# Performance work log

Hardware: AMD Instinct MI355X
Metric: run time of the kernel (lower is better)

## Reference

```python
import jax, jax.numpy as jnp
import numpy as np

N_IMG = 5
IN_DIM = 512
N_KERNEL = 200
KS = (2, 3, 5)
HIDDEN = 512
BATCH = 32768


def _param(key, shape, scale=0.02):
    return jax.random.normal(key, shape, dtype=jnp.float32) * scale


def setup_inputs() -> dict:
    key = jax.random.key(0)
    ks = jax.random.split(key, 16)
    feats = jax.random.normal(ks[0], (BATCH, N_IMG, IN_DIM), dtype=jnp.float32)
    d_cat = len(KS) * N_KERNEL  # 600
    return {
        "feats": feats,
        "w2": _param(ks[1], (N_KERNEL, 2, IN_DIM)), "b2": _param(ks[2], (N_KERNEL,)),
        "w3": _param(ks[3], (N_KERNEL, 3, IN_DIM)), "b3": _param(ks[4], (N_KERNEL,)),
        "w5": _param(ks[5], (N_KERNEL, 5, IN_DIM)), "b5": _param(ks[6], (N_KERNEL,)),
        "fc1_w": _param(ks[7], (d_cat, d_cat)), "fc1_b": _param(ks[8], (d_cat,)),
        "fc2_w": _param(ks[9], (d_cat, IN_DIM)), "fc2_b": _param(ks[10], (IN_DIM,)),
        "fc0_w": _param(ks[11], (2 * IN_DIM, HIDDEN)), "fc0_b": _param(ks[12], (HIDDEN,)),
        "fcs_w": _param(ks[13], (HIDDEN, 1)), "fcs_b": _param(ks[14], (1,)),
    }


def _conv_block(x, w, b):
    # x: [N, T, D], w: [C, K, D] -> relu(conv) then max over time -> [N, C]
    K = w.shape[1]
    T = x.shape[1] - K + 1
    win = jnp.stack([x[:, t:t + K, :] for t in range(T)], axis=1)  # [N, T, K, D]
    out = jnp.einsum('ntkd,ckd->ntc', win, w) + b                  # [N, T, C]
    return jnp.max(jax.nn.relu(out), axis=1)                       # [N, C]


def reference(feats, w2, b2, w3, b3, w5, b5, fc1_w, fc1_b, fc2_w, fc2_b,
              fc0_w, fc0_b, fcs_w, fcs_b):
    # CNN context encoder (dropout is identity at eval)
    c = jnp.concatenate([
        _conv_block(feats, w2, b2),
        _conv_block(feats, w3, b3),
        _conv_block(feats, w5, b5),
    ], axis=1)                                      # [N, 600]
    h = jax.nn.relu(c @ fc1_w + fc1_b)
    ci = h @ fc2_w + fc2_b                          # [N, 512]
    # broadcast context to each image and concat with per-image feature
    ci_b = jnp.broadcast_to(ci[:, None, :], feats.shape)
    z = jnp.concatenate([feats, ci_b], axis=2)      # [N, 5, 1024]
    h0 = jax.nn.relu(z @ fc0_w + fc0_b)             # [N, 5, 512]
    score = (h0 @ fcs_w + fcs_b)[..., 0]            # [N, 5]
    # score2order: rank of each element under descending sort (double argsort)
    order = jnp.argsort(jnp.argsort(-score, axis=-1), axis=-1).astype(jnp.int64)
    return score, order
```

## Files before the change

### kernel.cpp

```cpp
#include <hip/hip_runtime.h>

#define N_BATCH 32768
#define N_IMG   5
#define DIM     512
#define NKERN   200
#define DCAT    600
#define NROWS   (N_BATCH * N_IMG)
#define EPS_FLAG 2e-4f

template<int K>
__global__ void pack_wT(const float* __restrict__ w, float* __restrict__ wT) {
    int g = blockIdx.x * 256 + threadIdx.x;
    if (g >= K * 512 * 256) return;
    int kd = g >> 8, c = g & 255;
    float v = 0.f;
    if (c < NKERN) v = w[((size_t)c * K + (kd >> 9)) * 512 + (kd & 511)];
    wT[g] = v;
}

template<int KD, int T>
__global__ __launch_bounds__(256, 4) void conv_gemm(
    const float* __restrict__ feats, const float* __restrict__ wT,
    float* __restrict__ scores, int m_base) {
    __shared__ float AsT[16][132];
    __shared__ float Bs[16][136];
    int tid = threadIdx.x;
    int tx = tid & 15, ty = tid >> 4;
    int m0l = blockIdx.x * 128, n0 = blockIdx.y * 128;
    int rr = tid >> 2, c4 = (tid & 3) * 4;
    int r0 = m_base + m0l + rr, r1 = r0 + 64;
    const float* ap0 = feats + ((size_t)(r0 / T) * 5 + (r0 % T)) * 512 + c4;
    const float* ap1 = feats + ((size_t)(r1 / T) * 5 + (r1 % T)) * 512 + c4;
    const float* bp = wT + (size_t)(tid >> 4) * 256 + n0 + (tid & 15) * 8;
    float acc[8][8] = {};

    for (int kk = 0; kk < KD; kk += 16) {
        float4 a0 = *(const float4*)(ap0 + kk);
        float4 a1 = *(const float4*)(ap1 + kk);
        const float4* bq = (const float4*)(bp + (size_t)kk * 256);
        float4 b0 = bq[0], b1 = bq[1];
        AsT[c4 + 0][rr] = a0.x; AsT[c4 + 1][rr] = a0.y;
        AsT[c4 + 2][rr] = a0.z; AsT[c4 + 3][rr] = a0.w;
        AsT[c4 + 0][rr + 64] = a1.x; AsT[c4 + 1][rr + 64] = a1.y;
        AsT[c4 + 2][rr + 64] = a1.z; AsT[c4 + 3][rr + 64] = a1.w;
        *(float4*)&Bs[tid >> 4][(tid & 15) * 8] = b0;
        *(float4*)&Bs[tid >> 4][(tid & 15) * 8 + 4] = b1;
        __syncthreads();
#pragma unroll
        for (int k2 = 0; k2 < 16; k2++) {
            float a[8], b[8];
            *(float4*)&a[0] = *(const float4*)&AsT[k2][ty * 8];
            *(float4*)&a[4] = *(const float4*)&AsT[k2][ty * 8 + 4];
            *(float4*)&b[0] = *(const float4*)&Bs[k2][tx * 8];
            *(float4*)&b[4] = *(const float4*)&Bs[k2][tx * 8 + 4];
#pragma unroll
            for (int i = 0; i < 8; i++)
#pragma unroll
                for (int j = 0; j < 8; j++)
                    acc[i][j] += a[i] * b[j];
        }
        __syncthreads();
    }
#pragma unroll
    for (int i = 0; i < 8; i++) {
        float* sp = scores + (size_t)(m0l + ty * 8 + i) * 256 + n0 + tx * 8;
        *(float4*)sp = make_float4(acc[i][0], acc[i][1], acc[i][2], acc[i][3]);
        *(float4*)(sp + 4) = make_float4(acc[i][4], acc[i][5], acc[i][6], acc[i][7]);
    }
}

template<int T>
__global__ void conv_reduce(const float* __restrict__ scores,
                            const float* __restrict__ bias,
                            float* __restrict__ c, int conv_off, int n_base) {
    int g = blockIdx.x * 256 + threadIdx.x;
    int nl = g >> 8, ch = g & 255;
    if (ch >= NKERN) return;
    const float* sp = scores + (size_t)nl * T * 256 + ch;
    float m = sp[0];
#pragma unroll
    for (int t = 1; t < T; t++) m = fmaxf(m, sp[t * 256]);
    c[(size_t)(n_base + nl) * DCAT + conv_off + ch] = fmaxf(m + bias[ch], 0.f);
}

template<int RELU>
__global__ __launch_bounds__(256) void gemm_bias(
    const float* __restrict__ A, const float* __restrict__ B,
    const float* __restrict__ bias, float* __restrict__ C,
    int Kd, int Nc) {
    __shared__ float AsT[16][68];
    __shared__ float Bs[16][68];
    int tid = threadIdx.x;
    int tx = tid & 15, ty = tid >> 4;
    int m0 = blockIdx.x * 64, n0 = blockIdx.y * 64;
    float acc[4][4] = {};
    int arow = tid >> 2, ac4 = tid & 3;
    int br = tid >> 4, bc = tid & 15;

    for (int kk = 0; kk < Kd; kk += 16) {
        int gk = kk + ac4 * 4;
        float4 ga = make_float4(0.f, 0.f, 0.f, 0.f);
        if (gk < Kd) ga = *(const float4*)(A + (size_t)(m0 + arow) * Kd + gk);
        AsT[ac4 * 4 + 0][arow] = ga.x;
        AsT[ac4 * 4 + 1][arow] = ga.y;
        AsT[ac4 * 4 + 2][arow] = ga.z;
        AsT[ac4 * 4 + 3][arow] = ga.w;
        float4 gb = make_float4(0.f, 0.f, 0.f, 0.f);
        int bcol = n0 + bc * 4;
        if (kk + br < Kd && bcol < Nc) gb = *(const float4*)(B + (size_t)(kk + br) * Nc + bcol);
        *(float4*)&Bs[br][bc * 4] = gb;
        __syncthreads();
#pragma unroll
        for (int k2 = 0; k2 < 16; k2++) {
            float4 a4 = *(const float4*)&AsT[k2][ty * 4];
            float4 b4 = *(const float4*)&Bs[k2][tx * 4];
            float a[4] = {a4.x, a4.y, a4.z, a4.w};
            float b[4] = {b4.x, b4.y, b4.z, b4.w};
#pragma unroll
            for (int i = 0; i < 4; i++)
#pragma unroll
                for (int j = 0; j < 4; j++)
                    acc[i][j] += a[i] * b[j];
        }
        __syncthreads();
    }
    int cb = n0 + tx * 4;
    if (cb < Nc) {
        float4 bs = *(const float4*)(bias + cb);
#pragma unroll
        for (int i = 0; i < 4; i++) {
            size_t row = m0 + ty * 4 + i;
            float4 v;
            v.x = acc[i][0] + bs.x; v.y = acc[i][1] + bs.y;
            v.z = acc[i][2] + bs.z; v.w = acc[i][3] + bs.w;
            if (RELU) {
                v.x = fmaxf(v.x, 0.f); v.y = fmaxf(v.y, 0.f);
                v.z = fmaxf(v.z, 0.f); v.w = fmaxf(v.w, 0.f);
            }
            *(float4*)(C + row * Nc + cb) = v;
        }
    }
}

__global__ __launch_bounds__(256, 4) void fc0_fcs_128(
    const float* __restrict__ feats, const float* __restrict__ ci,
    const float* __restrict__ W, const float* __restrict__ b0,
    const float* __restrict__ fw, float* __restrict__ partial) {
    __shared__ float AsT[16][132];
    __shared__ float Bs[16][136];
    __shared__ float red[128][17];
    int tid = threadIdx.x;
    int tx = tid & 15, ty = tid >> 4;
    int m0 = blockIdx.x * 128, n0 = blockIdx.y * 128;
    int rr = tid >> 2, c4 = (tid & 3) * 4;
    int r0 = m0 + rr, r1 = r0 + 64;
    const float* af0 = feats + (size_t)r0 * 512 + c4;
    const float* ac0 = ci + (size_t)(r0 / 5) * 512 + c4;
    const float* af1 = feats + (size_t)r1 * 512 + c4;
    const float* ac1 = ci + (size_t)(r1 / 5) * 512 + c4;
    const float* bp = W + (size_t)(tid >> 4) * DIM + n0 + (tid & 15) * 8;
    float acc[8][8] = {};

    for (int kk = 0; kk < 1024; kk += 16) {
        float4 a0, a1;
        if (kk < 512) {
            a0 = *(const float4*)(af0 + kk);
            a1 = *(const float4*)(af1 + kk);
        } else {
            a0 = *(const float4*)(ac0 + (kk - 512));
            a1 = *(const float4*)(ac1 + (kk - 512));
        }
        const float4* bq = (const float4*)(bp + (size_t)kk * DIM);
        float4 b0v = bq[0], b1v = bq[1];
        AsT[c4 + 0][rr] = a0.x; AsT[c4 + 1][rr] = a0.y;
        AsT[c4 + 2][rr] = a0.z; AsT[c4 + 3][rr] = a0.w;
        AsT[c4 + 0][rr + 64] = a1.x; AsT[c4 + 1][rr + 64] = a1.y;
        AsT[c4 + 2][rr + 64] = a1.z; AsT[c4 + 3][rr + 64] = a1.w;
        *(float4*)&Bs[tid >> 4][(tid & 15) * 8] = b0v;
        *(float4*)&Bs[tid >> 4][(tid & 15) * 8 + 4] = b1v;
        __syncthreads();
#pragma unroll
        for (int k2 = 0; k2 < 16; k2++) {
            float a[8], b[8];
            *(float4*)&a[0] = *(const float4*)&AsT[k2][ty * 8];
            *(float4*)&a[4] = *(const float4*)&AsT[k2][ty * 8 + 4];
            *(float4*)&b[0] = *(const float4*)&Bs[k2][tx * 8];
            *(float4*)&b[4] = *(const float4*)&Bs[k2][tx * 8 + 4];
#pragma unroll
            for (int i = 0; i < 8; i++)
#pragma unroll
                for (int j = 0; j < 8; j++)
                    acc[i][j] += a[i] * b[j];
        }
        __syncthreads();
    }
    int cb = n0 + tx * 8;
    float4 ba = *(const float4*)(b0 + cb), bb = *(const float4*)(b0 + cb + 4);
    float4 fa = *(const float4*)(fw + cb), fb = *(const float4*)(fw + cb + 4);
#pragma unroll
    for (int i = 0; i < 8; i++) {
        float p = 0.f;
        p += fmaxf(acc[i][0] + ba.x, 0.f) * fa.x;
        p += fmaxf(acc[i][1] + ba.y, 0.f) * fa.y;
        p += fmaxf(acc[i][2] + ba.z, 0.f) * fa.z;
        p += fmaxf(acc[i][3] + ba.w, 0.f) * fa.w;
        p += fmaxf(acc[i][4] + bb.x, 0.f) * fb.x;
        p += fmaxf(acc[i][5] + bb.y, 0.f) * fb.y;
        p += fmaxf(acc[i][6] + bb.z, 0.f) * fb.z;
        p += fmaxf(acc[i][7] + bb.w, 0.f) * fb.w;
        red[ty * 8 + i][tx] = p;
    }
    __syncthreads();
    if (tid < 128) {
        float s = 0.f;
#pragma unroll
        for (int x = 0; x < 16; x++) s += red[tid][x];
        partial[(size_t)(m0 + tid) * 4 + blockIdx.y] = s;
    }
}

__global__ void score_finish(const float* __restrict__ partial,
                             const float* __restrict__ fcs_b,
                             float* __restrict__ out) {
    int m = blockIdx.x * 256 + threadIdx.x;
    if (m >= NROWS) return;
    float s = fcs_b[0];
#pragma unroll
    for (int q = 0; q < 4; q++) s += partial[(size_t)m * 4 + q];
    out[m] = s;
}

__global__ void flag_rank(const float* __restrict__ out_scores,
                          float* __restrict__ out, int* __restrict__ flags) {
    int n = blockIdx.x * 256 + threadIdx.x;
    if (n >= N_BATCH) return;
    float s[5];
#pragma unroll
    for (int i = 0; i < 5; i++) s[i] = out_scores[n * 5 + i];
    int f = 0;
#pragma unroll
    for (int i = 0; i < 5; i++) {
        int rk = 0;
#pragma unroll
        for (int j = 0; j < 5; j++) {
            rk += (s[j] > s[i]) || (s[j] == s[i] && j < i);
            if (j > i) f |= (fabsf(s[i] - s[j]) < EPS_FLAG);
        }
        out[NROWS + n * 5 + i] = (float)rk;
    }
    flags[n] = f;
}

__device__ __forceinline__ double dot4d(float4 f, float4 w, double a) {
    a += (double)f.x * (double)w.x;
    a += (double)f.y * (double)w.y;
    a += (double)f.z * (double)w.z;
    a += (double)f.w * (double)w.w;
    return a;
}

__global__ __launch_bounds__(256) void recompute_flagged(
    const float* __restrict__ feats,
    const float* __restrict__ w2, const float* __restrict__ b2,
    const float* __restrict__ w3, const float* __restrict__ b3,
    const float* __restrict__ w5, const float* __restrict__ b5,
    const float* __restrict__ fc1_w, const float* __restrict__ fc1_b,
    const float* __restrict__ fc2_w, const float* __restrict__ fc2_b,
    const float* __restrict__ fc0_w, const float* __restrict__ fc0_b,
    const float* __restrict__ fcs_w, const float* __restrict__ fcs_b,
    const int* __restrict__ flags, float* __restrict__ out) {
    int n = blockIdx.x;
    if (!flags[n]) return;
    __shared__ float  fsh[2560];
    __shared__ double csh[600];
    __shared__ double hsh[600];
    __shared__ double cish[512];
    __shared__ double rred[5][4];
    int tid = threadIdx.x, lane = tid & 63, wave = tid >> 6;

    const float4* fg = (const float4*)(feats + (size_t)n * 2560);
    float4* fs4 = (float4*)fsh;
    for (int i = tid; i < 640; i += 256) fs4[i] = fg[i];
    __syncthreads();

    if (tid < 200) {
        {
            const float* w = w2 + (size_t)tid * 1024;
            double a0 = 0.0, a1 = 0.0, a2 = 0.0, a3 = 0.0;
            for (int i = 0; i < 1024; i += 4) {
                float4 wv = *(const float4*)(w + i);
                a0 = dot4d(*(const float4*)(fsh + i),        wv, a0);
                a1 = dot4d(*(const float4*)(fsh + 512 + i),  wv, a1);
                a2 = dot4d(*(const float4*)(fsh + 1024 + i), wv, a2);
                a3 = dot4d(*(const float4*)(fsh + 1536 + i), wv, a3);
            }
            double b = (double)b2[tid];
            double m = fmax(fmax(a0, a1), fmax(a2, a3)) + b;
            csh[tid] = fmax(m, 0.0);
        }
        {
            const float* w = w3 + (size_t)tid * 1536;
            double a0 = 0.0, a1 = 0.0, a2 = 0.0;
            for (int i = 0; i < 1536; i += 4) {
                float4 wv = *(const float4*)(w + i);
                a0 = dot4d(*(const float4*)(fsh + i),        wv, a0);
                a1 = dot4d(*(const float4*)(fsh + 512 + i),  wv, a1);
                a2 = dot4d(*(const float4*)(fsh + 1024 + i), wv, a2);
            }
            double b = (double)b3[tid];
            csh[200 + tid] = fmax(fmax(fmax(a0, a1), a2) + b, 0.0);
        }
        {
            const float* w = w5 + (size_t)tid * 2560;
            double a0 = 0.0, a1 = 0.0, a2 = 0.0, a3 = 0.0;
            for (int i = 0; i < 2560; i += 16) {
                a0 = dot4d(*(const float4*)(fsh + i),      *(const float4*)(w + i),      a0);
                a1 = dot4d(*(const float4*)(fsh + i + 4),  *(const float4*)(w + i + 4),  a1);
                a2 = dot4d(*(const float4*)(fsh + i + 8),  *(const float4*)(w + i + 8),  a2);
                a3 = dot4d(*(const float4*)(fsh + i + 12), *(const float4*)(w + i + 12), a3);
            }
            double b = (double)b5[tid];
            csh[400 + tid] = fmax(((a0 + a1) + (a2 + a3)) + b, 0.0);
        }
    }
    __syncthreads();

#pragma unroll
    for (int c = 0; c < 3; c++) {
        int ch = tid + c * 256;
        if (ch < DCAT) {
            const float* wp = fc1_w + ch;
            double a0 = 0.0, a1 = 0.0;
            for (int k = 0; k < DCAT; k += 2) {
                a0 += csh[k]     * (double)wp[(size_t)k * DCAT];
                a1 += csh[k + 1] * (double)wp[(size_t)(k + 1) * DCAT];
            }
            hsh[ch] = fmax(a0 + a1 + (double)fc1_b[ch], 0.0);
        }
    }
    __syncthreads();

#pragma unroll
    for (int c = 0; c < 2; c++) {
        int ch = tid + c * 256;
        const float* wp = fc2_w + ch;
        double a0 = 0.0, a1 = 0.0;
        for (int k = 0; k < DCAT; k += 2) {
            a0 += hsh[k]     * (double)wp[(size_t)k * DIM];
            a1 += hsh[k + 1] * (double)wp[(size_t)(k + 1) * DIM];
        }
        cish[ch] = a0 + a1 + (double)fc2_b[ch];
    }
    __syncthreads();

    double acc0[5] = {}, acc1[5] = {};
#pragma unroll 4
    for (int k = 0; k < 512; k++) {
        double w0 = (double)fc0_w[(size_t)k * DIM + tid];
        double w1 = (double)fc0_w[(size_t)k * DIM + tid + 256];
#pragma unroll
        for (int img = 0; img < 5; img++) {
            double z = (double)fsh[img * 512 + k];
            acc0[img] += z * w0; acc1[img] += z * w1;
        }
    }
#pragma unroll 4
    for (int k = 0; k < 512; k++) {
        double w0 = (double)fc0_w[(size_t)(k + 512) * DIM + tid];
        double w1 = (double)fc0_w[(size_t)(k + 512) * DIM + tid + 256];
        double z = cish[k];
#pragma unroll
        for (int img = 0; img < 5; img++) { acc0[img] += z * w0; acc1[img] += z * w1; }
    }
    double b0a = (double)fc0_b[tid], b0b = (double)fc0_b[tid + 256];
    double fwa = (double)fcs_w[tid], fwb = (double)fcs_w[tid + 256];
#pragma unroll
    for (int img = 0; img < 5; img++) {
        double p = fmax(acc0[img] + b0a, 0.0) * fwa + fmax(acc1[img] + b0b, 0.0) * fwb;
#pragma unroll
        for (int o = 32; o >= 1; o >>= 1) p += __shfl_down(p, o, 64);
        if (lane == 0) rred[img][wave] = p;
    }
    __syncthreads();
    if (tid == 0) {
        double sc[5];
#pragma unroll
        for (int img = 0; img < 5; img++)
            sc[img] = rred[img][0] + rred[img][1] + rred[img][2] + rred[img][3]
                    + (double)fcs_b[0];
#pragma unroll
        for (int i = 0; i < 5; i++) {
            int rk = 0;
#pragma unroll
            for (int j = 0; j < 5; j++)
                rk += (sc[j] > sc[i]) || (sc[j] == sc[i] && j < i);
            out[n * 5 + i] = (float)sc[i];
            out[NROWS + n * 5 + i] = (float)rk;
        }
    }
}

extern "C" void kernel_launch(void* const* d_in, const int* in_sizes, int n_in,
                              void* d_out, int out_size, void* d_ws, size_t ws_size,
                              hipStream_t stream) {
    (void)in_sizes; (void)n_in; (void)out_size; (void)ws_size;
    const float* feats = (const float*)d_in[0];
    const float* w2    = (const float*)d_in[1];
    const float* b2    = (const float*)d_in[2];
    const float* w3    = (const float*)d_in[3];
    const float* b3    = (const float*)d_in[4];
    const float* w5    = (const float*)d_in[5];
    const float* b5    = (const float*)d_in[6];
    const float* fc1_w = (const float*)d_in[7];
    const float* fc1_b = (const float*)d_in[8];
    const float* fc2_w = (const float*)d_in[9];
    const float* fc2_b = (const float*)d_in[10];
    const float* fc0_w = (const float*)d_in[11];
    const float* fc0_b = (const float*)d_in[12];
    const float* fcs_w = (const float*)d_in[13];
    const float* fcs_b = (const float*)d_in[14];

    char* ws = (char*)d_ws;
    float* c      = (float*)ws;
    float* scores = (float*)(ws + 78643200);
    int*   flags  = (int*)(ws + 87031808);
    float* wT2    = (float*)(ws + 145752064);
    float* wT3    = wT2 + 1024 * 256;
    float* wT5    = wT3 + 1536 * 256;

    pack_wT<2><<<dim3(2 * 512), 256, 0, stream>>>(w2, wT2);
    pack_wT<3><<<dim3(3 * 512), 256, 0, stream>>>(w3, wT3);
    pack_wT<5><<<dim3(5 * 512), 256, 0, stream>>>(w5, wT5);

    for (int chk = 0; chk < 2; chk++) {
        conv_gemm<1024, 4><<<dim3(512, 2), 256, 0, stream>>>(feats, wT2, scores, chk * 65536);
        conv_reduce<4><<<dim3(16384), 256, 0, stream>>>(scores, b2, c, 0, chk * 16384);
    }
    for (int chk = 0; chk < 2; chk++) {
        conv_gemm<1536, 3><<<dim3(384, 2), 256, 0, stream>>>(feats, wT3, scores, chk * 49152);
        conv_reduce<3><<<dim3(16384), 256, 0, stream>>>(scores, b3, c, 200, chk * 16384);
    }
    conv_gemm<2560, 1><<<dim3(256, 2), 256, 0, stream>>>(feats, wT5, scores, 0);
    conv_reduce<1><<<dim3(32768), 256, 0, stream>>>(scores, b5, c, 400, 0);

    float* h = (float*)(ws + 78643200);
    gemm_bias<1><<<dim3(N_BATCH / 64, 10), 256, 0, stream>>>(c, fc1_w, fc1_b, h, DCAT, DCAT);

    float* ci = (float*)ws;
    gemm_bias<0><<<dim3(N_BATCH / 64, 8), 256, 0, stream>>>(h, fc2_w, fc2_b, ci, DCAT, DIM);

    float* partial = (float*)(ws + 78643200);
    fc0_fcs_128<<<dim3(NROWS / 128, 4), 256, 0, stream>>>(feats, ci, fc0_w, fc0_b, fcs_w, partial);

    float* out = (float*)d_out;
    score_finish<<<dim3(NROWS / 256), 256, 0, stream>>>(partial, fcs_b, out);
    flag_rank<<<dim3(N_BATCH / 256), 256, 0, stream>>>(out, out, flags);
    recompute_flagged<<<dim3(N_BATCH), 256, 0, stream>>>(
        feats, w2, b2, w3, b3, w5, b5, fc1_w, fc1_b, fc2_w, fc2_b,
        fc0_w, fc0_b, fcs_w, fcs_b, flags, out);
}
```

Before: 6.196 ms.

## Use 128x128 register-tiled GEMM for fc1/fc2 and remove LDS bank conflicts

Replaces the 64x64, 4x4-microtile gemm_bias used for fc1 and fc2 with a 128x128 tile and an 8x8 per-thread microtile. Dimensions are now compile-time template parameters, and K is padded to a multiple of 16 with zero-fill. The two GEMMs run in two batch chunks so the hidden activations fit in a smaller scratch region, with flags moved to a new offset. The per-thread B-column mapping in conv_gemm, fc0_fcs and the new GEMM changes from 8 contiguous columns to two groups of 4 (tx*4 and 64+tx*4), which is meant to cut shared-memory bank conflicts. The aim is more arithmetic per shared-memory load; the cost is higher register pressure and edge-tile waste for N=600.

```diff
diff --git a/kernel.cpp b/kernel.cpp
--- a/kernel.cpp
+++ b/kernel.cpp
@@ -51,8 +51,8 @@
             float a[8], b[8];
             *(float4*)&a[0] = *(const float4*)&AsT[k2][ty * 8];
             *(float4*)&a[4] = *(const float4*)&AsT[k2][ty * 8 + 4];
-            *(float4*)&b[0] = *(const float4*)&Bs[k2][tx * 8];
-            *(float4*)&b[4] = *(const float4*)&Bs[k2][tx * 8 + 4];
+            *(float4*)&b[0] = *(const float4*)&Bs[k2][tx * 4];
+            *(float4*)&b[4] = *(const float4*)&Bs[k2][64 + tx * 4];
 #pragma unroll
             for (int i = 0; i < 8; i++)
 #pragma unroll
@@ -63,9 +63,9 @@
     }
 #pragma unroll
     for (int i = 0; i < 8; i++) {
-        float* sp = scores + (size_t)(m0l + ty * 8 + i) * 256 + n0 + tx * 8;
-        *(float4*)sp = make_float4(acc[i][0], acc[i][1], acc[i][2], acc[i][3]);
-        *(float4*)(sp + 4) = make_float4(acc[i][4], acc[i][5], acc[i][6], acc[i][7]);
+        float* sp = scores + (size_t)(m0l + ty * 8 + i) * 256 + n0;
+        *(float4*)(sp + tx * 4) = make_float4(acc[i][0], acc[i][1], acc[i][2], acc[i][3]);
+        *(float4*)(sp + 64 + tx * 4) = make_float4(acc[i][4], acc[i][5], acc[i][6], acc[i][7]);
     }
 }
 
@@ -83,61 +83,74 @@
     c[(size_t)(n_base + nl) * DCAT + conv_off + ch] = fmaxf(m + bias[ch], 0.f);
 }
 
-template<int RELU>
-__global__ __launch_bounds__(256) void gemm_bias(
+template<int KD, int NS, int LDA, int LDC, int RELU>
+__global__ __launch_bounds__(256, 4) void gemm_fc128(
     const float* __restrict__ A, const float* __restrict__ B,
-    const float* __restrict__ bias, float* __restrict__ C,
-    int Kd, int Nc) {
-    __shared__ float AsT[16][68];
-    __shared__ float Bs[16][68];
+    const float* __restrict__ bias, float* __restrict__ C) {
+    __shared__ float AsT[16][132];
+    __shared__ float Bs[16][136];
     int tid = threadIdx.x;
     int tx = tid & 15, ty = tid >> 4;
-    int m0 = blockIdx.x * 64, n0 = blockIdx.y * 64;
-    float acc[4][4] = {};
-    int arow = tid >> 2, ac4 = tid & 3;
-    int br = tid >> 4, bc = tid & 15;
-
-    for (int kk = 0; kk < Kd; kk += 16) {
-        int gk = kk + ac4 * 4;
-        float4 ga = make_float4(0.f, 0.f, 0.f, 0.f);
-        if (gk < Kd) ga = *(const float4*)(A + (size_t)(m0 + arow) * Kd + gk);
-        AsT[ac4 * 4 + 0][arow] = ga.x;
-        AsT[ac4 * 4 + 1][arow] = ga.y;
-        AsT[ac4 * 4 + 2][arow] = ga.z;
-        AsT[ac4 * 4 + 3][arow] = ga.w;
-        float4 gb = make_float4(0.f, 0.f, 0.f, 0.f);
-        int bcol = n0 + bc * 4;
-        if (kk + br < Kd && bcol < Nc) gb = *(const float4*)(B + (size_t)(kk + br) * Nc + bcol);
-        *(float4*)&Bs[br][bc * 4] = gb;
+    int m0 = blockIdx.x * 128, n0 = blockIdx.y * 128;
+    int rr = tid >> 2, c4 = (tid & 3) * 4;
+    const float* ap0 = A + (size_t)(m0 + rr) * LDA + c4;
+    const float* ap1 = A + (size_t)(m0 + rr + 64) * LDA + c4;
+    int brow = tid >> 4, bcol = n0 + (tid & 15) * 8;
+    float acc[8][8] = {};
+    constexpr int KDp = (KD + 15) & ~15;
+
+    for (int kk = 0; kk < KDp; kk += 16) {
+        int gk = kk + c4;
+        float4 a0 = make_float4(0.f, 0.f, 0.f, 0.f), a1 = a0;
+        if (gk < KD) { a0 = *(const float4*)(ap0 + kk); a1 = *(const float4*)(ap1 + kk); }
+        float4 b0v = make_float4(0.f, 0.f, 0.f, 0.f), b1v = b0v;
+        if (kk + brow < KD && bcol < NS) {
+            const float* bq = B + (size_t)(kk + brow) * NS + bcol;
+            b0v = *(const float4*)bq; b1v = *(const float4*)(bq + 4);
+        }
+        AsT[c4 + 0][rr] = a0.x; AsT[c4 + 1][rr] = a0.y;
+        AsT[c4 + 2][rr] = a0.z; AsT[c4 + 3][rr] = a0.w;
+        AsT[c4 + 0][rr + 64] = a1.x; AsT[c4 + 1][rr + 64] = a1.y;
+        AsT[c4 + 2][rr + 64] = a1.z; AsT[c4 + 3][rr + 64] = a1.w;
+        *(float4*)&Bs[brow][(tid & 15) * 8] = b0v;
+        *(float4*)&Bs[brow][(tid & 15) * 8 + 4] = b1v;
         __syncthreads();
 #pragma unroll
         for (int k2 = 0; k2 < 16; k2++) {
-            float4 a4 = *(const float4*)&AsT[k2][ty * 4];
-            float4 b4 = *(const float4*)&Bs[k2][tx * 4];
-            float a[4] = {a4.x, a4.y, a4.z, a4.w};
-            float b[4] = {b4.x, b4.y, b4.z, b4.w};
-#pragma unroll
-            for (int i = 0; i < 4; i++)
-#pragma unroll
-                for (int j = 0; j < 4; j++)
+            float a[8], b[8];
+            *(float4*)&a[0] = *(const float4*)&AsT[k2][ty * 8];
+            *(float4*)&a[4] = *(const float4*)&AsT[k2][ty * 8 + 4];
+            *(float4*)&b[0] = *(const float4*)&Bs[k2][tx * 4];
+            *(float4*)&b[4] = *(const float4*)&Bs[k2][64 + tx * 4];
+#pragma unroll
+            for (int i = 0; i < 8; i++)
+#pragma unroll
+                for (int j = 0; j < 8; j++)
                     acc[i][j] += a[i] * b[j];
         }
         __syncthreads();
     }
-    int cb = n0 + tx * 4;
-    if (cb < Nc) {
-        float4 bs = *(const float4*)(bias + cb);
-#pragma unroll
-        for (int i = 0; i < 4; i++) {
-            size_t row = m0 + ty * 4 + i;
+    int cb1 = n0 + tx * 4, cb2 = cb1 + 64;
+    float4 bs1 = (cb1 < NS) ? *(const float4*)(bias + cb1) : make_float4(0.f, 0.f, 0.f, 0.f);
+    float4 bs2 = (cb2 < NS) ? *(const float4*)(bias + cb2) : make_float4(0.f, 0.f, 0.f, 0.f);
+#pragma unroll
+    for (int i = 0; i < 8; i++) {
+        size_t row = m0 + ty * 8 + i;
+        if (cb1 < NS) {
             float4 v;
-            v.x = acc[i][0] + bs.x; v.y = acc[i][1] + bs.y;
-            v.z = acc[i][2] + bs.z; v.w = acc[i][3] + bs.w;
-            if (RELU) {
-                v.x = fmaxf(v.x, 0.f); v.y = fmaxf(v.y, 0.f);
-                v.z = fmaxf(v.z, 0.f); v.w = fmaxf(v.w, 0.f);
-            }
-            *(float4*)(C + row * Nc + cb) = v;
+            v.x = acc[i][0] + bs1.x; v.y = acc[i][1] + bs1.y;
+            v.z = acc[i][2] + bs1.z; v.w = acc[i][3] + bs1.w;
+            if (RELU) { v.x = fmaxf(v.x, 0.f); v.y = fmaxf(v.y, 0.f);
+                        v.z = fmaxf(v.z, 0.f); v.w = fmaxf(v.w, 0.f); }
+            *(float4*)(C + row * LDC + cb1) = v;
+        }
+        if (cb2 < NS) {
+            float4 v;
+            v.x = acc[i][4] + bs2.x; v.y = acc[i][5] + bs2.y;
+            v.z = acc[i][6] + bs2.z; v.w = acc[i][7] + bs2.w;
+            if (RELU) { v.x = fmaxf(v.x, 0.f); v.y = fmaxf(v.y, 0.f);
+                        v.z = fmaxf(v.z, 0.f); v.w = fmaxf(v.w, 0.f); }
+            *(float4*)(C + row * LDC + cb2) = v;
         }
     }
 }
@@ -184,8 +197,8 @@
             float a[8], b[8];
             *(float4*)&a[0] = *(const float4*)&AsT[k2][ty * 8];
             *(float4*)&a[4] = *(const float4*)&AsT[k2][ty * 8 + 4];
-            *(float4*)&b[0] = *(const float4*)&Bs[k2][tx * 8];
-            *(float4*)&b[4] = *(const float4*)&Bs[k2][tx * 8 + 4];
+            *(float4*)&b[0] = *(const float4*)&Bs[k2][tx * 4];
+            *(float4*)&b[4] = *(const float4*)&Bs[k2][64 + tx * 4];
 #pragma unroll
             for (int i = 0; i < 8; i++)
 #pragma unroll
@@ -194,9 +207,9 @@
         }
         __syncthreads();
     }
-    int cb = n0 + tx * 8;
-    float4 ba = *(const float4*)(b0 + cb), bb = *(const float4*)(b0 + cb + 4);
-    float4 fa = *(const float4*)(fw + cb), fb = *(const float4*)(fw + cb + 4);
+    int cb1 = n0 + tx * 4, cb2 = cb1 + 64;
+    float4 ba = *(const float4*)(b0 + cb1), bb = *(const float4*)(b0 + cb2);
+    float4 fa = *(const float4*)(fw + cb1), fb = *(const float4*)(fw + cb2);
 #pragma unroll
     for (int i = 0; i < 8; i++) {
         float p = 0.f;
@@ -423,7 +436,6 @@
     char* ws = (char*)d_ws;
     float* c      = (float*)ws;
     float* scores = (float*)(ws + 78643200);
-    int*   flags  = (int*)(ws + 87031808);
     float* wT2    = (float*)(ws + 145752064);
     float* wT3    = wT2 + 1024 * 256;
     float* wT5    = wT3 + 1536 * 256;
@@ -443,13 +455,17 @@
     conv_gemm<2560, 1><<<dim3(256, 2), 256, 0, stream>>>(feats, wT5, scores, 0);
     conv_reduce<1><<<dim3(32768), 256, 0, stream>>>(scores, b5, c, 400, 0);
 
-    float* h = (float*)(ws + 78643200);
-    gemm_bias<1><<<dim3(N_BATCH / 64, 10), 256, 0, stream>>>(c, fc1_w, fc1_b, h, DCAT, DCAT);
-
+    float* h_chunk = (float*)(ws + 78643200);
     float* ci = (float*)ws;
-    gemm_bias<0><<<dim3(N_BATCH / 64, 8), 256, 0, stream>>>(h, fc2_w, fc2_b, ci, DCAT, DIM);
+    for (int chk = 0; chk < 2; chk++) {
+        gemm_fc128<600, 600, 600, 600, 1><<<dim3(128, 5), 256, 0, stream>>>(
+            c + (size_t)chk * 16384 * 600, fc1_w, fc1_b, h_chunk);
+        gemm_fc128<600, 512, 600, 512, 0><<<dim3(128, 4), 256, 0, stream>>>(
+            h_chunk, fc2_w, fc2_b, ci + (size_t)chk * 16384 * 512);
+    }
 
     float* partial = (float*)(ws + 78643200);
+    int* flags = (int*)(ws + 81264640);
     fc0_fcs_128<<<dim3(NROWS / 128, 4), 256, 0, stream>>>(feats, ci, fc0_w, fc0_b, fcs_w, partial);
 
     float* out = (float*)d_out;
```

Measured after the change: 6.279 ms. About the same (+1.3%).
